# Kernel optimization log

Measured on AMD Instinct MI355X. Metric: run time of the kernel, lower is better.

The kernel has to match this reference:

```python
import jax, jax.numpy as jnp
import numpy as np
import math

N = 32768       # v_len * w_len
E = 262144
NFEAT = 512
NHID = 256
NCLASS = 40
DEPTH = 2
EPS = 0.1
PRUNE_FACTOR = 0.25


def setup_inputs() -> dict:
    key = jax.random.key(0)
    ks = jax.random.split(key, 8)
    x = jax.random.normal(ks[0], (N, NFEAT), jnp.float32)
    edge_index = jax.random.randint(ks[1], (2, E), 0, N, dtype=jnp.int64)
    edge_attr = jax.random.uniform(ks[2], (E,), jnp.float32)
    W_start = jax.random.normal(ks[3], (NHID, NFEAT), jnp.float32) / np.sqrt(NFEAT)
    b_start = jnp.zeros((NHID,), jnp.float32)
    # FAConv att_l/att_r are Linear(channels, 1, bias=False); one pair per layer
    att_l = jax.random.normal(ks[4], (DEPTH, NHID), jnp.float32) / np.sqrt(NHID)
    att_r = jax.random.normal(ks[5], (DEPTH, NHID), jnp.float32) / np.sqrt(NHID)
    W_end = jax.random.normal(ks[6], (NCLASS, NHID), jnp.float32) / np.sqrt(NHID)
    b_end = jnp.zeros((NCLASS,), jnp.float32)
    return {"x": x, "edge_index": edge_index, "edge_attr": edge_attr,
            "W_start": W_start, "b_start": b_start, "att_l": att_l,
            "att_r": att_r, "W_end": W_end, "b_end": b_end,
            "v_len": 1024, "w_len": 32}


def _forward(x, edge_attr, W_start, b_start, att_l, att_r, W_end, b_end,
             edge_index, v_len, w_len):
    src, dst = edge_index[0], edge_index[1]
    h = jax.nn.relu(x @ W_start.T + b_start)   # [N, nhid]
    h0 = h
    n = h.shape[0]
    top_idx = jnp.ones((n,), h.dtype)           # node keep-mask
    edge_mask = jnp.ones((edge_attr.shape[0],), h.dtype)  # subgraph() as edge mask
    col_off = jnp.arange(w_len)
    for l in range(DEPTH):
        # FAConv: out[i] = eps*h0[i] + sum_j w_ij * tanh(att_l.h[j] + att_r.h[i]) * h[j]
        al = h @ att_l[l]                       # [N]
        ar = h @ att_r[l]                       # [N]
        alpha = jnp.tanh(al[src] + ar[dst])     # [E]
        w = edge_attr * edge_mask
        msgs = h[src] * (alpha * w)[:, None]    # [E, nhid]
        agg = jax.ops.segment_sum(msgs, dst, num_segments=n)
        h = agg + EPS * h0
        # pruning: zero previously dropped nodes, rank by norm within each column
        h = h * top_idx[:, None]
        norm_h = jax.lax.stop_gradient(jnp.linalg.norm(h, axis=1)).reshape(v_len, w_len)
        order = jnp.argsort(-norm_h, axis=0)    # descending per column
        drop_from = math.ceil(v_len * (PRUNE_FACTOR / (l + 1)))
        drop_idx = order[drop_from:, :]         # rows to drop, per column
        flat_idx = (drop_idx * w_len + col_off).reshape(-1)
        top_idx = top_idx.at[flat_idx].set(0.0)
        # subgraph(): drop every edge touching a pruned node (== zero its weight)
        edge_mask = edge_mask * top_idx[src] * top_idx[dst]
        h = h * top_idx[:, None]
    out = h @ W_end.T + b_end
    return out * top_idx[:, None]


def reference(x, edge_index, edge_attr, W_start, b_start, att_l, att_r,
              W_end, b_end, v_len, w_len):
    return _forward(x, edge_attr, W_start, b_start, att_l, att_r, W_end, b_end,
                    edge_index, v_len, w_len)
```

## Files before the change

kernel.cpp:

```cpp
#include <hip/hip_runtime.h>
#include <math.h>

#define N_NODES 32768
#define E_EDGES 262144
#define NFEAT   512
#define NHID    256
#define NCLASS  40
#define EPSV    0.1f
#define VLEN    1024
#define WLEN    32
#define KEEP0   256
#define KEEP1   128

typedef __attribute__((ext_vector_type(8)))  short bf16x8;
typedef __attribute__((ext_vector_type(4)))  float f32x4;
typedef __attribute__((ext_vector_type(16))) float f32x16;
typedef __attribute__((ext_vector_type(4)))  int   i32x4;
typedef __attribute__((ext_vector_type(8)))  unsigned short us8;

__device__ inline unsigned short f2bf(float f) {
    unsigned int u = __builtin_bit_cast(unsigned int, f);
    return (unsigned short)((u + 0x7FFFu + ((u >> 16) & 1u)) >> 16);
}
__device__ inline float bf2f(unsigned short h) {
    unsigned int u = ((unsigned int)h) << 16;
    return __builtin_bit_cast(float, u);
}

__device__ inline void split_pair(float a, float b, unsigned& hi, unsigned& lo) {
    unsigned ua = __builtin_bit_cast(unsigned, a);
    unsigned ub = __builtin_bit_cast(unsigned, b);
    unsigned ha = ua & 0xFFFF0000u, hb = ub & 0xFFFF0000u;
    hi = (ha >> 16) | hb;
    float la = a - __builtin_bit_cast(float, ha);
    float lb = b - __builtin_bit_cast(float, hb);
    unsigned ula = __builtin_bit_cast(unsigned, la);
    unsigned ulb = __builtin_bit_cast(unsigned, lb);
    lo = (ula >> 16) | (ulb & 0xFFFF0000u);
}

__device__ __forceinline__ void gload16(const void* g, void* l) {
    __builtin_amdgcn_global_load_lds(
        (const __attribute__((address_space(1))) unsigned int*)g,
        (__attribute__((address_space(3))) unsigned int*)l,
        16, 0, 0);
}

__global__ __launch_bounds__(256) void prep_count_kernel(
        float* __restrict__ top, const float* __restrict__ Ws,
        unsigned short* __restrict__ Whi, unsigned short* __restrict__ Wlo,
        float* __restrict__ al0ar0, const int* __restrict__ dst,
        int* __restrict__ cnt) {
    int blk = blockIdx.x;
    int tid = threadIdx.x;
    if (blk < 128) {
        top[blk * 256 + tid] = 1.0f;
    } else if (blk < 256) {
        int j = (blk - 128) * 256 + tid;
        float4 v = ((const float4*)Ws)[j];
        ushort4 hh, ll;
        hh.x = f2bf(v.x); ll.x = f2bf(v.x - bf2f(hh.x));
        hh.y = f2bf(v.y); ll.y = f2bf(v.y - bf2f(hh.y));
        hh.z = f2bf(v.z); ll.z = f2bf(v.z - bf2f(hh.z));
        hh.w = f2bf(v.w); ll.w = f2bf(v.w - bf2f(hh.w));
        ((ushort4*)Whi)[j] = hh;
        ((ushort4*)Wlo)[j] = ll;
    } else if (blk < 512) {
        al0ar0[(blk - 256) * 256 + tid] = 0.f;
    } else {
        int e = (blk - 512) * 256 + tid;
        atomicAdd(&cnt[dst[e]], 1);
    }
}

__global__ __launch_bounds__(1024) void scan_kernel(const int* __restrict__ cnt,
                                                    int* __restrict__ off) {
    __shared__ int part[1024];
    int t = threadIdx.x;
    int4 c4[8];
#pragma unroll
    for (int i = 0; i < 8; ++i) c4[i] = ((const int4*)cnt)[t * 8 + i];
    int local[32];
    int s = 0;
#pragma unroll
    for (int i = 0; i < 8; ++i) {
        local[i*4+0] = s; s += c4[i].x;
        local[i*4+1] = s; s += c4[i].y;
        local[i*4+2] = s; s += c4[i].z;
        local[i*4+3] = s; s += c4[i].w;
    }
    part[t] = s;
    __syncthreads();
    for (int d = 1; d < 1024; d <<= 1) {
        int v = (t >= d) ? part[t - d] : 0;
        __syncthreads();
        part[t] += v;
        __syncthreads();
    }
    int prev = (t == 0) ? 0 : part[t - 1];
#pragma unroll
    for (int i = 0; i < 8; ++i) {
        int4 o;
        o.x = prev + local[i*4+0];
        o.y = prev + local[i*4+1];
        o.z = prev + local[i*4+2];
        o.w = prev + local[i*4+3];
        ((int4*)off)[t * 8 + i] = o;
    }
    if (t == 1023) off[N_NODES] = prev + s;
}

__global__ __launch_bounds__(512, 4) void gemm_scatter(
        const float* __restrict__ x, const unsigned short* __restrict__ Whi,
        const unsigned short* __restrict__ Wlo, const float* __restrict__ b,
        float* __restrict__ h0,
        const float* __restrict__ attl0, const float* __restrict__ attr0,
        float* __restrict__ al0, float* __restrict__ ar0,
        const int* __restrict__ srcp, const int* __restrict__ dstp,
        const float* __restrict__ eattr, const int* __restrict__ off_,
        int* __restrict__ cur_, int* __restrict__ csr_src, float* __restrict__ csr_w) {
    __shared__ float          As[2][128 * 32];
    __shared__ unsigned short Bhs[2][128 * 32];
    __shared__ unsigned short Bls[2][128 * 32];

    if (blockIdx.x < 512) {
        int e = blockIdx.x * 512 + threadIdx.x;
        int d = dstp[e];
        int p = atomicAdd(&cur_[d], 1);
        int k = off_[d] + p;
        csr_src[k] = srcp[e];
        csr_w[k]   = eattr[e];
        return;
    }

    int bid  = blockIdx.x - 512;
    int tid  = threadIdx.x;
    int wid  = tid >> 6;
    int lane = tid & 63;
    int l31  = lane & 31;
    int khalf = lane >> 5;
    int wr = wid >> 1, wc = wid & 1;

    int wg = (bid & 7) * 64 + (bid >> 3);
    int row0 = (wg >> 1) * 128;
    int col0 = (wg & 1) * 128;

    f32x16 acc[2];
#pragma unroll
    for (int nr = 0; nr < 2; ++nr)
#pragma unroll
        for (int e = 0; e < 16; ++e) acc[nr][e] = 0.f;

    auto stage = [&](int kt, int buf) {
#pragma unroll
        for (int i = 0; i < 2; ++i) {
            int c    = wid * 2 + i;
            int d    = c * 1024 + lane * 16;
            int row  = d >> 7;
            int off  = d & 127;
            int loff = off ^ ((row & 7) << 4);
            const float* src = &x[(size_t)(row0 + row) * NFEAT + kt * 32 + (loff >> 2)];
            gload16(src, &As[buf][c * 256]);
        }
        {
            int d     = wid * 1024 + lane * 16;
            int wrow  = d >> 6;
            int slot  = (d >> 4) & 3;
            int lslot = slot ^ ((wrow >> 1) & 3);
            size_t so = (size_t)(col0 + wrow) * NFEAT + kt * 32 + lslot * 8;
            gload16(&Whi[so], &Bhs[buf][wid * 512]);
            gload16(&Wlo[so], &Bls[buf][wid * 512]);
        }
    };

    stage(0, 0);
    __syncthreads();

    for (int kt = 0; kt < NFEAT / 32; ++kt) {
        int cur = kt & 1;
        if (kt + 1 < NFEAT / 32) stage(kt + 1, cur ^ 1);

        const float*          Ab  = As[cur];
        const unsigned short* Bhb = Bhs[cur];
        const unsigned short* Blb = Bls[cur];

#pragma unroll
        for (int s = 0; s < 2; ++s) {
            int rt = wr * 32 + l31;
            const char* rowp = (const char*)(Ab + rt * 32);
            int lo0 = s * 64 + khalf * 32;
            int sw  = (rt & 7) << 4;
            f32x4 va = *(const f32x4*)(rowp + (lo0 ^ sw));
            f32x4 vb = *(const f32x4*)(rowp + ((lo0 + 16) ^ sw));
            unsigned h01, h23, h45, h67, l01, l23, l45, l67;
            split_pair(va[0], va[1], h01, l01);
            split_pair(va[2], va[3], h23, l23);
            split_pair(vb[0], vb[1], h45, l45);
            split_pair(vb[2], vb[3], h67, l67);
            i32x4 hv = {(int)h01, (int)h23, (int)h45, (int)h67};
            i32x4 lv = {(int)l01, (int)l23, (int)l45, (int)l67};
            bf16x8 ah  = __builtin_bit_cast(bf16x8, hv);
            bf16x8 alo = __builtin_bit_cast(bf16x8, lv);

            bf16x8 bh[2], bl[2];
#pragma unroll
            for (int nr = 0; nr < 2; ++nr) {
                int ct = wc * 64 + nr * 32 + l31;
                int lb = s * 32 + khalf * 16;
                int ob = lb ^ (((ct >> 1) & 3) << 4);
                bh[nr] = *(const bf16x8*)((const char*)(Bhb + ct * 32) + ob);
                bl[nr] = *(const bf16x8*)((const char*)(Blb + ct * 32) + ob);
            }
#pragma unroll
            for (int nr = 0; nr < 2; ++nr) {
                acc[nr] = __builtin_amdgcn_mfma_f32_32x32x16_bf16(ah,  bh[nr], acc[nr], 0, 0, 0);
                acc[nr] = __builtin_amdgcn_mfma_f32_32x32x16_bf16(ah,  bl[nr], acc[nr], 0, 0, 0);
                acc[nr] = __builtin_amdgcn_mfma_f32_32x32x16_bf16(alo, bh[nr], acc[nr], 0, 0, 0);
            }
        }
        __syncthreads();
    }

    float biasv[2], attlv[2], attrv[2];
    int colv[2];
#pragma unroll
    for (int nr = 0; nr < 2; ++nr) {
        colv[nr]  = col0 + wc * 64 + nr * 32 + l31;
        biasv[nr] = b[colv[nr]];
        attlv[nr] = attl0[colv[nr]];
        attrv[nr] = attr0[colv[nr]];
    }
#pragma unroll
    for (int r = 0; r < 16; ++r) {
        int rowt = (r & 3) + 8 * (r >> 2) + 4 * khalf;
        int row = row0 + wr * 32 + rowt;
        float dl = 0.f, dr = 0.f;
#pragma unroll
        for (int nr = 0; nr < 2; ++nr) {
            float v = acc[nr][r] + biasv[nr];
            v = v > 0.f ? v : 0.f;
            h0[(size_t)row * NHID + colv[nr]] = v;
            dl += v * attlv[nr];
            dr += v * attrv[nr];
        }
#pragma unroll
        for (int m = 1; m <= 16; m <<= 1) {
            dl += __shfl_xor(dl, m);
            dr += __shfl_xor(dr, m);
        }
        if (l31 == 0) {
            atomicAdd(&al0[row], dl);
            atomicAdd(&ar0[row], dr);
        }
    }
}

__global__ __launch_bounds__(256) void gather_l0(
        const int* __restrict__ csr_src, const int* __restrict__ off,
        const float* __restrict__ csr_w,
        const float* __restrict__ al0, const float* __restrict__ ar0,
        const float* __restrict__ h0,
        float* __restrict__ h_out, float* __restrict__ nrm,
        const float* __restrict__ attl1, const float* __restrict__ attr1,
        float* __restrict__ al1, float* __restrict__ ar1) {
    int node = blockIdx.x * 4 + (threadIdx.x >> 6);
    int lane = threadIdx.x & 63;
    size_t base = (size_t)node * NHID + lane * 4;
    float arn = ar0[node];
    int k0 = off[node], k1 = off[node + 1];
    float4 a1 = make_float4(0.f, 0.f, 0.f, 0.f);
    float4 a2 = make_float4(0.f, 0.f, 0.f, 0.f);
    for (int cbase = k0; cbase < k1; cbase += 64) {
        int nk = k1 - cbase; if (nk > 64) nk = 64;
        float cv = 0.f; int sv = 0;
        if (lane < nk) {
            int kk = cbase + lane;
            sv = csr_src[kk];
            cv = tanhf(al0[sv] + arn) * csr_w[kk];
        }
        int j = 0;
        for (; j + 7 < nk; j += 8) {
            float c0=__shfl(cv,j),   c1=__shfl(cv,j+1), c2=__shfl(cv,j+2), c3=__shfl(cv,j+3);
            float c4=__shfl(cv,j+4), c5=__shfl(cv,j+5), c6=__shfl(cv,j+6), c7=__shfl(cv,j+7);
            int   s0=__shfl(sv,j),   s1=__shfl(sv,j+1), s2=__shfl(sv,j+2), s3=__shfl(sv,j+3);
            int   s4=__shfl(sv,j+4), s5=__shfl(sv,j+5), s6=__shfl(sv,j+6), s7=__shfl(sv,j+7);
            float4 v0 = *(const float4*)&h0[(size_t)s0 * NHID + lane * 4];
            float4 v1 = *(const float4*)&h0[(size_t)s1 * NHID + lane * 4];
            float4 v2 = *(const float4*)&h0[(size_t)s2 * NHID + lane * 4];
            float4 v3 = *(const float4*)&h0[(size_t)s3 * NHID + lane * 4];
            float4 v4 = *(const float4*)&h0[(size_t)s4 * NHID + lane * 4];
            float4 v5 = *(const float4*)&h0[(size_t)s5 * NHID + lane * 4];
            float4 v6 = *(const float4*)&h0[(size_t)s6 * NHID + lane * 4];
            float4 v7 = *(const float4*)&h0[(size_t)s7 * NHID + lane * 4];
            a1.x += c0*v0.x + c1*v1.x + c2*v2.x + c3*v3.x;
            a1.y += c0*v0.y + c1*v1.y + c2*v2.y + c3*v3.y;
            a1.z += c0*v0.z + c1*v1.z + c2*v2.z + c3*v3.z;
            a1.w += c0*v0.w + c1*v1.w + c2*v2.w + c3*v3.w;
            a2.x += c4*v4.x + c5*v5.x + c6*v6.x + c7*v7.x;
            a2.y += c4*v4.y + c5*v5.y + c6*v6.y + c7*v7.y;
            a2.z += c4*v4.z + c5*v5.z + c6*v6.z + c7*v7.z;
            a2.w += c4*v4.w + c5*v5.w + c6*v6.w + c7*v7.w;
        }
        for (; j + 3 < nk; j += 4) {
            float c0=__shfl(cv,j), c1=__shfl(cv,j+1), c2=__shfl(cv,j+2), c3=__shfl(cv,j+3);
            int   s0=__shfl(sv,j), s1=__shfl(sv,j+1), s2=__shfl(sv,j+2), s3=__shfl(sv,j+3);
            float4 v0 = *(const float4*)&h0[(size_t)s0 * NHID + lane * 4];
            float4 v1 = *(const float4*)&h0[(size_t)s1 * NHID + lane * 4];
            float4 v2 = *(const float4*)&h0[(size_t)s2 * NHID + lane * 4];
            float4 v3 = *(const float4*)&h0[(size_t)s3 * NHID + lane * 4];
            a1.x += c0*v0.x + c1*v1.x + c2*v2.x + c3*v3.x;
            a1.y += c0*v0.y + c1*v1.y + c2*v2.y + c3*v3.y;
            a1.z += c0*v0.z + c1*v1.z + c2*v2.z + c3*v3.z;
            a1.w += c0*v0.w + c1*v1.w + c2*v2.w + c3*v3.w;
        }
        for (; j < nk; ++j) {
            float c = __shfl(cv, j);
            int   s = __shfl(sv, j);
            float4 v = *(const float4*)&h0[(size_t)s * NHID + lane * 4];
            a1.x += c*v.x; a1.y += c*v.y; a1.z += c*v.z; a1.w += c*v.w;
        }
    }
    float4 z = *(const float4*)&h0[base];
    float4 v;
    v.x = a1.x + a2.x + EPSV * z.x;
    v.y = a1.y + a2.y + EPSV * z.y;
    v.z = a1.z + a2.z + EPSV * z.z;
    v.w = a1.w + a2.w + EPSV * z.w;
    *(float4*)&h_out[base] = v;
    float ss = v.x * v.x + v.y * v.y + v.z * v.z + v.w * v.w;
    float4 lv = *(const float4*)&attl1[lane * 4];
    float4 rv = *(const float4*)&attr1[lane * 4];
    float sl = v.x * lv.x + v.y * lv.y + v.z * lv.z + v.w * lv.w;
    float sr = v.x * rv.x + v.y * rv.y + v.z * rv.z + v.w * rv.w;
#pragma unroll
    for (int o = 32; o; o >>= 1) {
        ss += __shfl_down(ss, o);
        sl += __shfl_down(sl, o);
        sr += __shfl_down(sr, o);
    }
    if (lane == 0) { nrm[node] = sqrtf(ss); al1[node] = sl; ar1[node] = sr; }
}

__global__ __launch_bounds__(256) void gather_l1(
        const int* __restrict__ surv, const int* __restrict__ csr_src,
        const int* __restrict__ off, const float* __restrict__ csr_w,
        const float* __restrict__ al1, const float* __restrict__ ar1,
        const float* __restrict__ top, const float* __restrict__ h_in,
        const float* __restrict__ h0,
        float* __restrict__ h_out, float* __restrict__ nrm) {
    int node = surv[blockIdx.x * 4 + (threadIdx.x >> 6)];
    int lane = threadIdx.x & 63;
    size_t base = (size_t)node * NHID + lane * 4;
    float arn = ar1[node];
    int k0 = off[node], k1 = off[node + 1];
    float4 acc = make_float4(0.f, 0.f, 0.f, 0.f);
    for (int cbase = k0; cbase < k1; cbase += 64) {
        int nk = k1 - cbase; if (nk > 64) nk = 64;
        float cv = 0.f; int sv = 0;
        if (lane < nk) {
            int kk = cbase + lane;
            sv = csr_src[kk];
            float w = csr_w[kk] * top[sv];
            cv = (w == 0.f) ? 0.f : tanhf(al1[sv] + arn) * w;
        }
        int j = 0;
        for (; j + 3 < nk; j += 4) {
            float c0 = __shfl(cv, j),     c1 = __shfl(cv, j + 1);
            float c2 = __shfl(cv, j + 2), c3 = __shfl(cv, j + 3);
            int   s0 = __shfl(sv, j),     s1 = __shfl(sv, j + 1);
            int   s2 = __shfl(sv, j + 2), s3 = __shfl(sv, j + 3);
            if (c0 != 0.f) { float4 v = *(const float4*)&h_in[(size_t)s0 * NHID + lane * 4];
                acc.x += c0 * v.x; acc.y += c0 * v.y; acc.z += c0 * v.z; acc.w += c0 * v.w; }
            if (c1 != 0.f) { float4 v = *(const float4*)&h_in[(size_t)s1 * NHID + lane * 4];
                acc.x += c1 * v.x; acc.y += c1 * v.y; acc.z += c1 * v.z; acc.w += c1 * v.w; }
            if (c2 != 0.f) { float4 v = *(const float4*)&h_in[(size_t)s2 * NHID + lane * 4];
                acc.x += c2 * v.x; acc.y += c2 * v.y; acc.z += c2 * v.z; acc.w += c2 * v.w; }
            if (c3 != 0.f) { float4 v = *(const float4*)&h_in[(size_t)s3 * NHID + lane * 4];
                acc.x += c3 * v.x; acc.y += c3 * v.y; acc.z += c3 * v.z; acc.w += c3 * v.w; }
        }
        for (; j < nk; ++j) {
            float c = __shfl(cv, j);
            if (c != 0.f) {
                int s = __shfl(sv, j);
                float4 v = *(const float4*)&h_in[(size_t)s * NHID + lane * 4];
                acc.x += c * v.x; acc.y += c * v.y; acc.z += c * v.z; acc.w += c * v.w;
            }
        }
    }
    float4 z = *(const float4*)&h0[base];
    float4 v;
    v.x = acc.x + EPSV * z.x;
    v.y = acc.y + EPSV * z.y;
    v.z = acc.z + EPSV * z.z;
    v.w = acc.w + EPSV * z.w;
    *(float4*)&h_out[base] = v;
    float ss = v.x * v.x + v.y * v.y + v.z * v.z + v.w * v.w;
#pragma unroll
    for (int o = 32; o; o >>= 1) ss += __shfl_down(ss, o);
    if (lane == 0) nrm[node] = sqrtf(ss);
}

__global__ __launch_bounds__(256) void topk_kernel(
        const float* __restrict__ nrm_in, float* __restrict__ nrm_out,
        float* __restrict__ top, int drop_from, int* __restrict__ surv) {
    __shared__ float s[VLEN];
    int c     = blockIdx.x >> 2;
    int chunk = blockIdx.x & 3;
    int t = threadIdx.x;
    for (int r = t; r < VLEN; r += 256) s[r] = nrm_in[r * WLEN + c];
    __syncthreads();
    int r = chunk * 256 + t;
    float v = s[r];
    int cnt = 0;
#pragma unroll 8
    for (int r2 = 0; r2 < VLEN; ++r2) {
        float v2 = s[r2];
        cnt += (v2 > v) || (v2 == v && r2 < r);
    }
    int idx = r * WLEN + c;
    if (cnt >= drop_from) {
        top[idx] = 0.f;
        nrm_out[idx] = 0.f;
    } else {
        surv[c * drop_from + cnt] = idx;
    }
}

#define ASTR 40
#define OBSTR 264
__global__ __launch_bounds__(256) void out_mfma_list(
        const int* __restrict__ surv2, const float* __restrict__ h,
        const float* __restrict__ We, const float* __restrict__ be,
        float* __restrict__ out) {
    __shared__ unsigned short Bh[48 * OBSTR];
    __shared__ unsigned short Bl[48 * OBSTR];
    __shared__ unsigned short Ah[64 * ASTR];
    __shared__ unsigned short Al[64 * ASTR];
    __shared__ int sids[64];
    int tid  = threadIdx.x;
    int w    = tid >> 6;
    int lane = tid & 63;
    int m16  = lane & 15;
    int kblk = lane >> 4;

    if (tid < 64) sids[tid] = surv2[blockIdx.x * 64 + tid];

    for (int i = tid; i < 48 * 64; i += 256) {
        int r = i >> 6, k4 = i & 63;
        float4 v = (r < NCLASS) ? *(const float4*)&We[r * NHID + k4 * 4]
                                : make_float4(0.f, 0.f, 0.f, 0.f);
        ushort4 hh, ll;
        hh.x = f2bf(v.x); ll.x = f2bf(v.x - bf2f(hh.x));
        hh.y = f2bf(v.y); ll.y = f2bf(v.y - bf2f(hh.y));
        hh.z = f2bf(v.z); ll.z = f2bf(v.z - bf2f(hh.z));
        hh.w = f2bf(v.w); ll.w = f2bf(v.w - bf2f(hh.w));
        *(ushort4*)&Bh[r * OBSTR + k4 * 4] = hh;
        *(ushort4*)&Bl[r * OBSTR + k4 * 4] = ll;
    }
    __syncthreads();

    f32x4 acc[3];
#pragma unroll
    for (int nr = 0; nr < 3; ++nr)
#pragma unroll
        for (int e = 0; e < 4; ++e) acc[nr][e] = 0.f;

    for (int kt = 0; kt < NHID; kt += 32) {
#pragma unroll
        for (int i = 0; i < 2; ++i) {
            int f = tid + 256 * i;
            int row = f >> 3, k4 = f & 7;
            int node = sids[row];
            float4 v = *(const float4*)&h[(size_t)node * NHID + kt + k4 * 4];
            ushort4 hh, ll;
            hh.x = f2bf(v.x); ll.x = f2bf(v.x - bf2f(hh.x));
            hh.y = f2bf(v.y); ll.y = f2bf(v.y - bf2f(hh.y));
            hh.z = f2bf(v.z); ll.z = f2bf(v.z - bf2f(hh.z));
            hh.w = f2bf(v.w); ll.w = f2bf(v.w - bf2f(hh.w));
            *(ushort4*)&Ah[row * ASTR + k4 * 4] = hh;
            *(ushort4*)&Al[row * ASTR + k4 * 4] = ll;
        }
        __syncthreads();
        int ar_ = w * 16 + m16;
        bf16x8 ah  = *(const bf16x8*)&Ah[ar_ * ASTR + kblk * 8];
        bf16x8 alo = *(const bf16x8*)&Al[ar_ * ASTR + kblk * 8];
#pragma unroll
        for (int nr = 0; nr < 3; ++nr) {
            int br = nr * 16 + m16;
            bf16x8 bh = *(const bf16x8*)&Bh[br * OBSTR + kt + kblk * 8];
            bf16x8 bl = *(const bf16x8*)&Bl[br * OBSTR + kt + kblk * 8];
            acc[nr] = __builtin_amdgcn_mfma_f32_16x16x32_bf16(ah,  bh, acc[nr], 0, 0, 0);
            acc[nr] = __builtin_amdgcn_mfma_f32_16x16x32_bf16(ah,  bl, acc[nr], 0, 0, 0);
            acc[nr] = __builtin_amdgcn_mfma_f32_16x16x32_bf16(alo, bh, acc[nr], 0, 0, 0);
        }
        __syncthreads();
    }
#pragma unroll
    for (int nr = 0; nr < 3; ++nr) {
        int col = nr * 16 + m16;
        if (col < NCLASS) {
            float bias = be[col];
#pragma unroll
            for (int r = 0; r < 4; ++r) {
                int row = w * 16 + kblk * 4 + r;
                int node = sids[row];
                out[(size_t)node * NCLASS + col] = acc[nr][r] + bias;
            }
        }
    }
}

extern "C" void kernel_launch(void* const* d_in, const int* in_sizes, int n_in,
                              void* d_out, int out_size, void* d_ws, size_t ws_size,
                              hipStream_t stream) {
    const float* x     = (const float*)d_in[0];
    const int*   ei    = (const int*)d_in[1];
    const float* eattr = (const float*)d_in[2];
    const float* Ws    = (const float*)d_in[3];
    const float* bs    = (const float*)d_in[4];
    const float* attl  = (const float*)d_in[5];
    const float* attr_ = (const float*)d_in[6];
    const float* We    = (const float*)d_in[7];
    const float* be    = (const float*)d_in[8];
    float* out = (float*)d_out;

    char* ws = (char*)d_ws;
    const size_t HB = (size_t)N_NODES * NHID * sizeof(float);
    float* hA  = (float*)(ws);
    float* hB  = (float*)(ws + HB);
    float* h0  = (float*)(ws + 2 * HB);
    char* sm = ws + 3 * HB;
    float* al0      = (float*)(sm);               sm += 131072;
    float* ar0      = (float*)(sm);               sm += 131072;
    float* al1      = (float*)(sm);               sm += 131072;
    float* ar1      = (float*)(sm);               sm += 131072;
    float* nrm      = (float*)(sm);               sm += 131072;
    float* top      = (float*)(sm);               sm += 131072;
    int*   cnt      = (int*)(sm);                 sm += 131072;
    int*   cur      = (int*)(sm);                 sm += 131072;
    int*   off      = (int*)(sm);                 sm += 262144;
    int*   csr_src  = (int*)(sm);                 sm += E_EDGES * 4;
    float* csr_w    = (float*)(sm);               sm += E_EDGES * 4;
    int*   surv0    = (int*)(sm);                 sm += KEEP0 * WLEN * 4;
    int*   surv2    = (int*)(sm);                 sm += KEEP1 * WLEN * 4;
    unsigned short* Whi = (unsigned short*)(sm);  sm += NHID * NFEAT * 2;
    unsigned short* Wlo = (unsigned short*)(sm);  sm += NHID * NFEAT * 2;

    const int* srcp = ei;
    const int* dstp = ei + E_EDGES;

    hipMemsetAsync(cnt, 0, 2 * 131072, stream);
    hipMemsetAsync(d_out, 0, (size_t)out_size * sizeof(float), stream);

    prep_count_kernel<<<1536, 256, 0, stream>>>(top, Ws, Whi, Wlo, al0, dstp, cnt);

    scan_kernel<<<1, 1024, 0, stream>>>(cnt, off);

    gemm_scatter<<<512 + 512, 512, 0, stream>>>(x, Whi, Wlo, bs, h0,
                                                attl, attr_, al0, ar0,
                                                srcp, dstp, eattr, off, cur,
                                                csr_src, csr_w);

    gather_l0<<<N_NODES / 4, 256, 0, stream>>>(csr_src, off, csr_w,
                                               al0, ar0, h0, hA, nrm,
                                               attl + NHID, attr_ + NHID, al1, ar1);
    topk_kernel<<<WLEN * 4, 256, 0, stream>>>(nrm, nrm, top, KEEP0, surv0);

    gather_l1<<<(KEEP0 * WLEN) / 4, 256, 0, stream>>>(surv0, csr_src, off, csr_w,
                                                      al1, ar1, top, hA, h0, hB, nrm);
    topk_kernel<<<WLEN * 4, 256, 0, stream>>>(nrm, nrm, top, KEEP1, surv2);

    out_mfma_list<<<(KEEP1 * WLEN) / 64, 256, 0, stream>>>(surv2, hB, We, be, out);
}
```

Baseline: 210.6 us.

## Split scatter from GEMM and process two nodes per wavefront in layer-0 gather

The CSR scatter, previously fused into the GEMM launch as extra blocks, becomes its own kernel, and the GEMM kernel now only computes h0 and the attention dot products. The layer-0 gather assigns two destination nodes to each wavefront and interleaves their neighbour loads, so more independent memory requests are in flight per wave. A fallback path handles nodes with more than 64 edges. The split adds a kernel launch and removes overlap between the scatter and the GEMM, and the dual-node loop uses more registers.

```diff
diff --git a/kernel.cpp b/kernel.cpp
--- a/kernel.cpp
+++ b/kernel.cpp
@@ -16,7 +16,6 @@
 typedef __attribute__((ext_vector_type(4)))  float f32x4;
 typedef __attribute__((ext_vector_type(16))) float f32x16;
 typedef __attribute__((ext_vector_type(4)))  int   i32x4;
-typedef __attribute__((ext_vector_type(8)))  unsigned short us8;
 
 __device__ inline unsigned short f2bf(float f) {
     unsigned int u = __builtin_bit_cast(unsigned int, f);
@@ -110,30 +109,28 @@
     if (t == 1023) off[N_NODES] = prev + s;
 }
 
-__global__ __launch_bounds__(512, 4) void gemm_scatter(
+__global__ void scatter_kernel(const int* __restrict__ src, const int* __restrict__ dst,
+                               const float* __restrict__ eattr,
+                               const int* __restrict__ off, int* __restrict__ cur,
+                               int* __restrict__ csr_src, float* __restrict__ csr_w) {
+    int e = blockIdx.x * 256 + threadIdx.x;
+    int d = dst[e];
+    int p = atomicAdd(&cur[d], 1);
+    int k = off[d] + p;
+    csr_src[k] = src[e];
+    csr_w[k]   = eattr[e];
+}
+
+__global__ __launch_bounds__(512, 4) void gemm_dots(
         const float* __restrict__ x, const unsigned short* __restrict__ Whi,
         const unsigned short* __restrict__ Wlo, const float* __restrict__ b,
         float* __restrict__ h0,
         const float* __restrict__ attl0, const float* __restrict__ attr0,
-        float* __restrict__ al0, float* __restrict__ ar0,
-        const int* __restrict__ srcp, const int* __restrict__ dstp,
-        const float* __restrict__ eattr, const int* __restrict__ off_,
-        int* __restrict__ cur_, int* __restrict__ csr_src, float* __restrict__ csr_w) {
+        float* __restrict__ al0, float* __restrict__ ar0) {
     __shared__ float          As[2][128 * 32];
     __shared__ unsigned short Bhs[2][128 * 32];
     __shared__ unsigned short Bls[2][128 * 32];
 
-    if (blockIdx.x < 512) {
-        int e = blockIdx.x * 512 + threadIdx.x;
-        int d = dstp[e];
-        int p = atomicAdd(&cur_[d], 1);
-        int k = off_[d] + p;
-        csr_src[k] = srcp[e];
-        csr_w[k]   = eattr[e];
-        return;
-    }
-
-    int bid  = blockIdx.x - 512;
     int tid  = threadIdx.x;
     int wid  = tid >> 6;
     int lane = tid & 63;
@@ -141,7 +138,7 @@
     int khalf = lane >> 5;
     int wr = wid >> 1, wc = wid & 1;
 
-    int wg = (bid & 7) * 64 + (bid >> 3);
+    int wg = (blockIdx.x & 7) * 64 + (blockIdx.x >> 3);
     int row0 = (wg >> 1) * 128;
     int col0 = (wg & 1) * 128;
 
@@ -263,82 +260,136 @@
         float* __restrict__ h_out, float* __restrict__ nrm,
         const float* __restrict__ attl1, const float* __restrict__ attr1,
         float* __restrict__ al1, float* __restrict__ ar1) {
-    int node = blockIdx.x * 4 + (threadIdx.x >> 6);
+    int sub  = threadIdx.x >> 6;
     int lane = threadIdx.x & 63;
-    size_t base = (size_t)node * NHID + lane * 4;
-    float arn = ar0[node];
-    int k0 = off[node], k1 = off[node + 1];
-    float4 a1 = make_float4(0.f, 0.f, 0.f, 0.f);
-    float4 a2 = make_float4(0.f, 0.f, 0.f, 0.f);
-    for (int cbase = k0; cbase < k1; cbase += 64) {
-        int nk = k1 - cbase; if (nk > 64) nk = 64;
-        float cv = 0.f; int sv = 0;
-        if (lane < nk) {
-            int kk = cbase + lane;
-            sv = csr_src[kk];
-            cv = tanhf(al0[sv] + arn) * csr_w[kk];
-        }
-        int j = 0;
-        for (; j + 7 < nk; j += 8) {
-            float c0=__shfl(cv,j),   c1=__shfl(cv,j+1), c2=__shfl(cv,j+2), c3=__shfl(cv,j+3);
-            float c4=__shfl(cv,j+4), c5=__shfl(cv,j+5), c6=__shfl(cv,j+6), c7=__shfl(cv,j+7);
-            int   s0=__shfl(sv,j),   s1=__shfl(sv,j+1), s2=__shfl(sv,j+2), s3=__shfl(sv,j+3);
-            int   s4=__shfl(sv,j+4), s5=__shfl(sv,j+5), s6=__shfl(sv,j+6), s7=__shfl(sv,j+7);
+    int nodeA = blockIdx.x * 8 + sub * 2;
+    int nodeB = nodeA + 1;
+    int kA0 = off[nodeA], kA1 = off[nodeA + 1], kB1 = off[nodeB + 1];
+    int nkA = kA1 - kA0, nkB = kB1 - kA1;
+    float arA = ar0[nodeA], arB = ar0[nodeB];
+    float4 aA = make_float4(0.f, 0.f, 0.f, 0.f);
+    float4 aB = make_float4(0.f, 0.f, 0.f, 0.f);
+
+    if (nkA <= 64 && nkB <= 64) {
+        float cvA = 0.f; int svA = 0;
+        if (lane < nkA) {
+            int kk = kA0 + lane;
+            svA = csr_src[kk];
+            cvA = tanhf(al0[svA] + arA) * csr_w[kk];
+        }
+        float cvB = 0.f; int svB = 0;
+        if (lane < nkB) {
+            int kk = kA1 + lane;
+            svB = csr_src[kk];
+            cvB = tanhf(al0[svB] + arB) * csr_w[kk];
+        }
+        int jA = 0, jB = 0;
+        while (jA + 3 < nkA && jB + 3 < nkB) {
+            int   sA0=__shfl(svA,jA),   sA1=__shfl(svA,jA+1), sA2=__shfl(svA,jA+2), sA3=__shfl(svA,jA+3);
+            int   sB0=__shfl(svB,jB),   sB1=__shfl(svB,jB+1), sB2=__shfl(svB,jB+2), sB3=__shfl(svB,jB+3);
+            float cA0=__shfl(cvA,jA),   cA1=__shfl(cvA,jA+1), cA2=__shfl(cvA,jA+2), cA3=__shfl(cvA,jA+3);
+            float cB0=__shfl(cvB,jB),   cB1=__shfl(cvB,jB+1), cB2=__shfl(cvB,jB+2), cB3=__shfl(cvB,jB+3);
+            float4 vA0 = *(const float4*)&h0[(size_t)sA0 * NHID + lane * 4];
+            float4 vA1 = *(const float4*)&h0[(size_t)sA1 * NHID + lane * 4];
+            float4 vA2 = *(const float4*)&h0[(size_t)sA2 * NHID + lane * 4];
+            float4 vA3 = *(const float4*)&h0[(size_t)sA3 * NHID + lane * 4];
+            float4 vB0 = *(const float4*)&h0[(size_t)sB0 * NHID + lane * 4];
+            float4 vB1 = *(const float4*)&h0[(size_t)sB1 * NHID + lane * 4];
+            float4 vB2 = *(const float4*)&h0[(size_t)sB2 * NHID + lane * 4];
+            float4 vB3 = *(const float4*)&h0[(size_t)sB3 * NHID + lane * 4];
+            aA.x += cA0*vA0.x + cA1*vA1.x + cA2*vA2.x + cA3*vA3.x;
+            aA.y += cA0*vA0.y + cA1*vA1.y + cA2*vA2.y + cA3*vA3.y;
+            aA.z += cA0*vA0.z + cA1*vA1.z + cA2*vA2.z + cA3*vA3.z;
+            aA.w += cA0*vA0.w + cA1*vA1.w + cA2*vA2.w + cA3*vA3.w;
+            aB.x += cB0*vB0.x + cB1*vB1.x + cB2*vB2.x + cB3*vB3.x;
+            aB.y += cB0*vB0.y + cB1*vB1.y + cB2*vB2.y + cB3*vB3.y;
+            aB.z += cB0*vB0.z + cB1*vB1.z + cB2*vB2.z + cB3*vB3.z;
+            aB.w += cB0*vB0.w + cB1*vB1.w + cB2*vB2.w + cB3*vB3.w;
+            jA += 4; jB += 4;
+        }
+        for (; jA + 3 < nkA; jA += 4) {
+            int   s0=__shfl(svA,jA), s1=__shfl(svA,jA+1), s2=__shfl(svA,jA+2), s3=__shfl(svA,jA+3);
+            float c0=__shfl(cvA,jA), c1=__shfl(cvA,jA+1), c2=__shfl(cvA,jA+2), c3=__shfl(cvA,jA+3);
             float4 v0 = *(const float4*)&h0[(size_t)s0 * NHID + lane * 4];
             float4 v1 = *(const float4*)&h0[(size_t)s1 * NHID + lane * 4];
             float4 v2 = *(const float4*)&h0[(size_t)s2 * NHID + lane * 4];
             float4 v3 = *(const float4*)&h0[(size_t)s3 * NHID + lane * 4];
-            float4 v4 = *(const float4*)&h0[(size_t)s4 * NHID + lane * 4];
-            float4 v5 = *(const float4*)&h0[(size_t)s5 * NHID + lane * 4];
-            float4 v6 = *(const float4*)&h0[(size_t)s6 * NHID + lane * 4];
-            float4 v7 = *(const float4*)&h0[(size_t)s7 * NHID + lane * 4];
-            a1.x += c0*v0.x + c1*v1.x + c2*v2.x + c3*v3.x;
-            a1.y += c0*v0.y + c1*v1.y + c2*v2.y + c3*v3.y;
-            a1.z += c0*v0.z + c1*v1.z + c2*v2.z + c3*v3.z;
-            a1.w += c0*v0.w + c1*v1.w + c2*v2.w + c3*v3.w;
-            a2.x += c4*v4.x + c5*v5.x + c6*v6.x + c7*v7.x;
-            a2.y += c4*v4.y + c5*v5.y + c6*v6.y + c7*v7.y;
-            a2.z += c4*v4.z + c5*v5.z + c6*v6.z + c7*v7.z;
-            a2.w += c4*v4.w + c5*v5.w + c6*v6.w + c7*v7.w;
-        }
-        for (; j + 3 < nk; j += 4) {
-            float c0=__shfl(cv,j), c1=__shfl(cv,j+1), c2=__shfl(cv,j+2), c3=__shfl(cv,j+3);
-            int   s0=__shfl(sv,j), s1=__shfl(sv,j+1), s2=__shfl(sv,j+2), s3=__shfl(sv,j+3);
+            aA.x += c0*v0.x + c1*v1.x + c2*v2.x + c3*v3.x;
+            aA.y += c0*v0.y + c1*v1.y + c2*v2.y + c3*v3.y;
+            aA.z += c0*v0.z + c1*v1.z + c2*v2.z + c3*v3.z;
+            aA.w += c0*v0.w + c1*v1.w + c2*v2.w + c3*v3.w;
+        }
+        for (; jA < nkA; ++jA) {
+            int s = __shfl(svA, jA); float c = __shfl(cvA, jA);
+            float4 v = *(const float4*)&h0[(size_t)s * NHID + lane * 4];
+            aA.x += c*v.x; aA.y += c*v.y; aA.z += c*v.z; aA.w += c*v.w;
+        }
+        for (; jB + 3 < nkB; jB += 4) {
+            int   s0=__shfl(svB,jB), s1=__shfl(svB,jB+1), s2=__shfl(svB,jB+2), s3=__shfl(svB,jB+3);
+            float c0=__shfl(cvB,jB), c1=__shfl(cvB,jB+1), c2=__shfl(cvB,jB+2), c3=__shfl(cvB,jB+3);
             float4 v0 = *(const float4*)&h0[(size_t)s0 * NHID + lane * 4];
             float4 v1 = *(const float4*)&h0[(size_t)s1 * NHID + lane * 4];
             float4 v2 = *(const float4*)&h0[(size_t)s2 * NHID + lane * 4];
             float4 v3 = *(const float4*)&h0[(size_t)s3 * NHID + lane * 4];
-            a1.x += c0*v0.x + c1*v1.x + c2*v2.x + c3*v3.x;
-            a1.y += c0*v0.y + c1*v1.y + c2*v2.y + c3*v3.y;
-            a1.z += c0*v0.z + c1*v1.z + c2*v2.z + c3*v3.z;
-            a1.w += c0*v0.w + c1*v1.w + c2*v2.w + c3*v3.w;
-        }
-        for (; j < nk; ++j) {
-            float c = __shfl(cv, j);
-            int   s = __shfl(sv, j);
+            aB.x += c0*v0.x + c1*v1.x + c2*v2.x + c3*v3.x;
+            aB.y += c0*v0.y + c1*v1.y + c2*v2.y + c3*v3.y;
+            aB.z += c0*v0.z + c1*v1.z + c2*v2.z + c3*v3.z;
+            aB.w += c0*v0.w + c1*v1.w + c2*v2.w + c3*v3.w;
+        }
+        for (; jB < nkB; ++jB) {
+            int s = __shfl(svB, jB); float c = __shfl(cvB, jB);
             float4 v = *(const float4*)&h0[(size_t)s * NHID + lane * 4];
-            a1.x += c*v.x; a1.y += c*v.y; a1.z += c*v.z; a1.w += c*v.w;
-        }
-    }
-    float4 z = *(const float4*)&h0[base];
-    float4 v;
-    v.x = a1.x + a2.x + EPSV * z.x;
-    v.y = a1.y + a2.y + EPSV * z.y;
-    v.z = a1.z + a2.z + EPSV * z.z;
-    v.w = a1.w + a2.w + EPSV * z.w;
-    *(float4*)&h_out[base] = v;
-    float ss = v.x * v.x + v.y * v.y + v.z * v.z + v.w * v.w;
-    float4 lv = *(const float4*)&attl1[lane * 4];
-    float4 rv = *(const float4*)&attr1[lane * 4];
-    float sl = v.x * lv.x + v.y * lv.y + v.z * lv.z + v.w * lv.w;
-    float sr = v.x * rv.x + v.y * rv.y + v.z * rv.z + v.w * rv.w;
-#pragma unroll
-    for (int o = 32; o; o >>= 1) {
-        ss += __shfl_down(ss, o);
-        sl += __shfl_down(sl, o);
-        sr += __shfl_down(sr, o);
-    }
-    if (lane == 0) { nrm[node] = sqrtf(ss); al1[node] = sl; ar1[node] = sr; }
+            aB.x += c*v.x; aB.y += c*v.y; aB.z += c*v.z; aB.w += c*v.w;
+        }
+    } else {
+        for (int which = 0; which < 2; ++which) {
+            int k0 = which ? kA1 : kA0;
+            int k1 = which ? kB1 : kA1;
+            float arn = which ? arB : arA;
+            float4 acc = make_float4(0.f, 0.f, 0.f, 0.f);
+            for (int cbase = k0; cbase < k1; cbase += 64) {
+                int nk = k1 - cbase; if (nk > 64) nk = 64;
+                float cv = 0.f; int sv = 0;
+                if (lane < nk) {
+                    int kk = cbase + lane;
+                    sv = csr_src[kk];
+                    cv = tanhf(al0[sv] + arn) * csr_w[kk];
+                }
+                for (int j = 0; j < nk; ++j) {
+                    int s = __shfl(sv, j); float c = __shfl(cv, j);
+                    float4 v = *(const float4*)&h0[(size_t)s * NHID + lane * 4];
+                    acc.x += c*v.x; acc.y += c*v.y; acc.z += c*v.z; acc.w += c*v.w;
+                }
+            }
+            if (which) aB = acc; else aA = acc;
+        }
+    }
+
+#pragma unroll
+    for (int which = 0; which < 2; ++which) {
+        int node = which ? nodeB : nodeA;
+        float4 a = which ? aB : aA;
+        size_t base = (size_t)node * NHID + lane * 4;
+        float4 z = *(const float4*)&h0[base];
+        float4 v;
+        v.x = a.x + EPSV * z.x;
+        v.y = a.y + EPSV * z.y;
+        v.z = a.z + EPSV * z.z;
+        v.w = a.w + EPSV * z.w;
+        *(float4*)&h_out[base] = v;
+        float ss = v.x * v.x + v.y * v.y + v.z * v.z + v.w * v.w;
+        float4 lv = *(const float4*)&attl1[lane * 4];
+        float4 rv = *(const float4*)&attr1[lane * 4];
+        float sl = v.x * lv.x + v.y * lv.y + v.z * lv.z + v.w * lv.w;
+        float sr = v.x * rv.x + v.y * rv.y + v.z * rv.z + v.w * rv.w;
+#pragma unroll
+        for (int o = 32; o; o >>= 1) {
+            ss += __shfl_down(ss, o);
+            sl += __shfl_down(sl, o);
+            sr += __shfl_down(sr, o);
+        }
+        if (lane == 0) { nrm[node] = sqrtf(ss); al1[node] = sl; ar1[node] = sr; }
+    }
 }
 
 __global__ __launch_bounds__(256) void gather_l1(
@@ -553,15 +604,14 @@
     hipMemsetAsync(d_out, 0, (size_t)out_size * sizeof(float), stream);
 
     prep_count_kernel<<<1536, 256, 0, stream>>>(top, Ws, Whi, Wlo, al0, dstp, cnt);
-
     scan_kernel<<<1, 1024, 0, stream>>>(cnt, off);
-
-    gemm_scatter<<<512 + 512, 512, 0, stream>>>(x, Whi, Wlo, bs, h0,
-                                                attl, attr_, al0, ar0,
-                                                srcp, dstp, eattr, off, cur,
-                                                csr_src, csr_w);
-
-    gather_l0<<<N_NODES / 4, 256, 0, stream>>>(csr_src, off, csr_w,
+    scatter_kernel<<<E_EDGES / 256, 256, 0, stream>>>(srcp, dstp, eattr, off, cur,
+                                                      csr_src, csr_w);
+
+    gemm_dots<<<N_NODES / 128 * 2, 512, 0, stream>>>(x, Whi, Wlo, bs, h0,
+                                                     attl, attr_, al0, ar0);
+
+    gather_l0<<<N_NODES / 8, 256, 0, stream>>>(csr_src, off, csr_w,
                                                al0, ar0, h0, hA, nrm,
                                                attl + NHID, attr_ + NHID, al1, ar1);
     topk_kernel<<<WLEN * 4, 256, 0, stream>>>(nrm, nrm, top, KEEP0, surv0);
```

Result: slower. 215.2 us (+2.2%).
